# Kernel tuning notes

Measured on AMD Instinct MI355X. Metric: run time of the kernel, lower is better.

Reference implementation:

```python
import jax, jax.numpy as jnp
import numpy as np

B, D, H = 32768, 256, 8
DH = D // H
SCALE = 1.0 / float(np.sqrt(DH))
# neighbor indices: for query node i, context = the other 3 nodes (in order)
NEIGH = np.array([[1, 2, 3], [0, 2, 3], [0, 1, 3], [0, 1, 2]], dtype=np.int32)


def setup_inputs() -> dict:
    key = jax.random.key(0)
    ks = jax.random.split(key, 6)
    s = 0.02
    mk = lambda k: jax.random.normal(k, (D, D), jnp.float32) * s
    return {
        "tokens": jax.random.normal(ks[0], (B, 4, D), jnp.float32),
        "Wq": mk(ks[1]),
        "Wk": mk(ks[2]),
        "Wv": mk(ks[3]),
        "Wr": mk(ks[4]),
        "Wo": mk(ks[5]),
        "ln_g": jnp.ones((D,), jnp.float32),
        "ln_b": jnp.zeros((D,), jnp.float32),
    }


def reference(tokens, Wq, Wk, Wv, Wr, Wo, ln_g, ln_b):
    # tokens: [B,4,D]. All 4 modality queries share one GCA block (share_gca=True),
    # so we batch the 4-node complete-graph message passing into one pass.
    neigh = jnp.asarray(NEIGH)
    ctx = tokens[:, neigh]                    # [B,4,3,D]
    Q = tokens @ Wq.T                         # [B,4,D]
    K = ctx @ Wk.T                            # [B,4,3,D]
    V = ctx @ Wv.T
    R = ctx @ Wr.T
    V_eff = jax.nn.sigmoid(R) * V             # gated values
    Qh = Q.reshape(B, 4, H, DH)
    Kh = K.reshape(B, 4, 3, H, DH)
    Vh = V_eff.reshape(B, 4, 3, H, DH)
    scores = jnp.einsum('bihd,bilhd->bihl', Qh, Kh) * SCALE   # [B,4,H,3]
    attn = jax.nn.softmax(scores, axis=-1)    # dropout = identity (eval mode)
    out = jnp.einsum('bihl,bilhd->bihd', attn, Vh).reshape(B, 4, D)
    out = out @ Wo.T
    y = tokens + out                          # residual
    mu = y.mean(-1, keepdims=True)
    var = y.var(-1, keepdims=True)
    y = (y - mu) / jnp.sqrt(var + 1e-5) * ln_g + ln_b   # LayerNorm
    # attn: [B,4,H,3] -> per-query attn maps (attn[:, i] == attn for modality-i query, [B,H,1,3] squeezed)
    return y, attn
```

## Files before the change

kernel.cpp:

```cpp
#include <hip/hip_runtime.h>
#include <stdint.h>


#define D_DIM   256
#define H_NUM   8
#define DH      32
#define RT      32
#define NTHR    512
#define ROWS_TOT 131072
#define Y_SZ    33554432
#define SCALE_F 0.17677669529663687f
#define W_ELEMS 65536
#define WS_NEED (5 * W_ELEMS * 2)

#define SX_LD   264
#define SQK_LD  776
#define KOFF    256
#define VOFF    512
#define SY_LD   260

typedef __attribute__((ext_vector_type(8))) short bf16x8;
typedef __attribute__((ext_vector_type(4))) float f32x4;

__device__ __forceinline__ float b2f(uint16_t s) {
    union { uint32_t u; float f; } c; c.u = ((uint32_t)s) << 16; return c.f;
}
__device__ __forceinline__ uint16_t f2b(float f) {
    union { float f; uint32_t u; } c; c.f = f;
    return (uint16_t)((c.u + 0x7fffu + ((c.u >> 16) & 1u)) >> 16);
}
__device__ __forceinline__ bf16x8 cvt8(const float* p) {
    const float4 a = *(const float4*)p;
    const float4 b = *(const float4*)(p + 4);
    bf16x8 r;
    r[0] = (short)f2b(a.x); r[1] = (short)f2b(a.y);
    r[2] = (short)f2b(a.z); r[3] = (short)f2b(a.w);
    r[4] = (short)f2b(b.x); r[5] = (short)f2b(b.y);
    r[6] = (short)f2b(b.z); r[7] = (short)f2b(b.w);
    return r;
}

__global__ __launch_bounds__(256)
void conv_weights(const float* __restrict__ Wq, const float* __restrict__ Wk,
                  const float* __restrict__ Wv, const float* __restrict__ Wr,
                  const float* __restrict__ Wo, uint16_t* __restrict__ dst)
{
    const int m = blockIdx.x >> 6;
    const float* src = (m == 0) ? Wq : (m == 1) ? Wk : (m == 2) ? Wv
                     : (m == 3) ? Wr : Wo;
    const int base = (blockIdx.x & 63) * 1024 + threadIdx.x * 4;
    const float4 v = *(const float4*)&src[base];
    uint2 pk;
    pk.x = (uint32_t)f2b(v.x) | ((uint32_t)f2b(v.y) << 16);
    pk.y = (uint32_t)f2b(v.z) | ((uint32_t)f2b(v.w) << 16);
    *(uint2*)&dst[(size_t)m * W_ELEMS + base] = pk;
}

template<bool WBF16>
__global__ __launch_bounds__(NTHR, 4)
void cmaa_fused(const float* __restrict__ tok,
                const float* __restrict__ Wq, const float* __restrict__ Wk,
                const float* __restrict__ Wv, const float* __restrict__ Wr,
                const float* __restrict__ Wo,
                const uint16_t* __restrict__ wbf,
                const float* __restrict__ lng, const float* __restrict__ lnb,
                float* __restrict__ outp)
{
    __shared__ __align__(16) uint16_t sX [RT * SX_LD];
    __shared__ __align__(16) uint16_t sQK[RT * SQK_LD];

    const int tid  = threadIdx.x;
    const int wv   = tid >> 6;
    const int lane = tid & 63;
    const int l15  = lane & 15;
    const int quad = lane >> 4;
    const int R0   = blockIdx.x * RT;
    const int koff = blockIdx.x & 7;

    {
        const float* g = tok + (size_t)R0 * D_DIM;
        #pragma unroll
        for (int t = tid; t < RT * (D_DIM / 8); t += NTHR) {
            const int row = t >> 5, c = t & 31;
            *(bf16x8*)&sX[row * SX_LD + c * 8] = cvt8(&g[row * D_DIM + c * 8]);
        }
    }
    __syncthreads();

    {
        const int  colbase = (((wv & 3) + blockIdx.x) & 3) * 64;
        const bool qk = (wv < 4);
        const float*    WF0 = qk ? Wq : Wv;
        const float*    WF1 = qk ? Wk : Wr;
        const uint16_t* WB0 = wbf + (size_t)(qk ? 0 : 2) * W_ELEMS;
        const uint16_t* WB1 = WB0 + W_ELEMS;

        f32x4 acc[2][2][4];
        #pragma unroll
        for (int m = 0; m < 2; ++m)
            #pragma unroll
            for (int mt = 0; mt < 2; ++mt)
                #pragma unroll
                for (int nt = 0; nt < 4; ++nt)
                    acc[m][mt][nt] = (f32x4){0.f, 0.f, 0.f, 0.f};

        #pragma unroll
        for (int i = 0; i < 8; ++i) {
            const int kk = (i + koff) & 7;
            const int k0 = kk * 32;
            bf16x8 a[2];
            #pragma unroll
            for (int mt = 0; mt < 2; ++mt)
                a[mt] = *(const bf16x8*)&sX[(mt * 16 + l15) * SX_LD + k0 + quad * 8];

            bf16x8 b0[4], b1[4];
            #pragma unroll
            for (int nt = 0; nt < 4; ++nt) {
                const int wrow = colbase + nt * 16 + l15;
                if constexpr (WBF16) {
                    b0[nt] = *(const bf16x8*)&WB0[(size_t)wrow * D_DIM + k0 + quad * 8];
                    b1[nt] = *(const bf16x8*)&WB1[(size_t)wrow * D_DIM + k0 + quad * 8];
                } else {
                    b0[nt] = cvt8(&WF0[(size_t)wrow * D_DIM + k0 + quad * 8]);
                    b1[nt] = cvt8(&WF1[(size_t)wrow * D_DIM + k0 + quad * 8]);
                }
            }
            #pragma unroll
            for (int nt = 0; nt < 4; ++nt)
                #pragma unroll
                for (int mt = 0; mt < 2; ++mt)
                    acc[0][mt][nt] = __builtin_amdgcn_mfma_f32_16x16x32_bf16(a[mt], b0[nt], acc[0][mt][nt], 0, 0, 0);
            #pragma unroll
            for (int nt = 0; nt < 4; ++nt)
                #pragma unroll
                for (int mt = 0; mt < 2; ++mt)
                    acc[1][mt][nt] = __builtin_amdgcn_mfma_f32_16x16x32_bf16(a[mt], b1[nt], acc[1][mt][nt], 0, 0, 0);
        }

        if (qk) {
            #pragma unroll
            for (int mt = 0; mt < 2; ++mt)
                #pragma unroll
                for (int nt = 0; nt < 4; ++nt)
                    #pragma unroll
                    for (int r = 0; r < 4; ++r) {
                        const int row = mt * 16 + quad * 4 + r;
                        const int col = colbase + nt * 16 + l15;
                        sQK[row * SQK_LD + col]        = f2b(acc[0][mt][nt][r]);
                        sQK[row * SQK_LD + KOFF + col] = f2b(acc[1][mt][nt][r]);
                    }
        } else {
            #pragma unroll
            for (int mt = 0; mt < 2; ++mt)
                #pragma unroll
                for (int nt = 0; nt < 4; ++nt)
                    #pragma unroll
                    for (int r = 0; r < 4; ++r) {
                        const int row = mt * 16 + quad * 4 + r;
                        const int col = colbase + nt * 16 + l15;
                        const float vvv = acc[0][mt][nt][r];
                        const float rr  = acc[1][mt][nt][r];
                        const float sig = 1.f / (1.f + __expf(-rr));
                        sQK[row * SQK_LD + VOFF + col] = f2b(vvv * sig);
                    }
        }
    }
    __syncthreads();

    const int wob = ((wv + blockIdx.x) & 7) * 32;
    bf16x8 bw3[2][8];
    {
        const uint16_t* WoB = wbf + (size_t)4 * W_ELEMS;
        #pragma unroll
        for (int nt = 0; nt < 2; ++nt) {
            const int worow = wob + nt * 16 + l15;
            #pragma unroll
            for (int i = 0; i < 8; ++i) {
                const int k0 = ((i + koff) & 7) * 32;
                if constexpr (WBF16)
                    bw3[nt][i] = *(const bf16x8*)&WoB[(size_t)worow * D_DIM + k0 + quad * 8];
                else
                    bw3[nt][i] = cvt8(&Wo[(size_t)worow * D_DIM + k0 + quad * 8]);
            }
        }
    }

    {
        const int r    = tid >> 4;
        const int h    = (tid >> 1) & 7;
        const int half = tid & 1;
        const int gr = R0 + r;
        const int i  = r & 3;
        const int rb = r & ~3;
        int rn[3];
        #pragma unroll
        for (int l = 0; l < 3; ++l) { const int jj = l + (l >= i); rn[l] = rb + jj; }
        const int qoff = h * DH + half * 16;

        float q[16];
        #pragma unroll
        for (int t = 0; t < 2; ++t) {
            const bf16x8 v = *(const bf16x8*)&sQK[r * SQK_LD + qoff + t * 8];
            #pragma unroll
            for (int j = 0; j < 8; ++j) q[t * 8 + j] = b2f((uint16_t)v[j]);
        }

        float sc[3];
        #pragma unroll
        for (int l = 0; l < 3; ++l) {
            float s = 0.f;
            #pragma unroll
            for (int t = 0; t < 2; ++t) {
                const bf16x8 v = *(const bf16x8*)&sQK[rn[l] * SQK_LD + KOFF + qoff + t * 8];
                #pragma unroll
                for (int j = 0; j < 8; ++j) s += q[t * 8 + j] * b2f((uint16_t)v[j]);
            }
            s += __shfl_xor(s, 1);
            sc[l] = s * SCALE_F;
        }
        const float mx = fmaxf(sc[0], fmaxf(sc[1], sc[2]));
        const float e0 = __expf(sc[0] - mx), e1 = __expf(sc[1] - mx), e2 = __expf(sc[2] - mx);
        const float inv = 1.f / (e0 + e1 + e2);
        const float al[3] = { e0 * inv, e1 * inv, e2 * inv };

        if (half == 0) {
            float* ap = outp + Y_SZ + ((size_t)gr * H_NUM + h) * 3;
            ap[0] = al[0]; ap[1] = al[1]; ap[2] = al[2];
        }

        #pragma unroll
        for (int t = 0; t < 2; ++t) {
            float o[8] = {0.f,0.f,0.f,0.f,0.f,0.f,0.f,0.f};
            #pragma unroll
            for (int l = 0; l < 3; ++l) {
                const bf16x8 vv = *(const bf16x8*)&sQK[rn[l] * SQK_LD + VOFF + qoff + t * 8];
                #pragma unroll
                for (int j = 0; j < 8; ++j) o[j] += al[l] * b2f((uint16_t)vv[j]);
            }
            bf16x8 pk;
            #pragma unroll
            for (int j = 0; j < 8; ++j) pk[j] = (short)f2b(o[j]);
            *(bf16x8*)&sQK[r * SQK_LD + qoff + t * 8] = pk;
        }
    }
    __syncthreads();

    {
        f32x4 acc3[2][2];
        #pragma unroll
        for (int mt = 0; mt < 2; ++mt)
            #pragma unroll
            for (int nt = 0; nt < 2; ++nt)
                acc3[mt][nt] = (f32x4){0.f, 0.f, 0.f, 0.f};

        #pragma unroll
        for (int i = 0; i < 8; ++i) {
            const int k0 = ((i + koff) & 7) * 32;
            bf16x8 a[2];
            #pragma unroll
            for (int mt = 0; mt < 2; ++mt)
                a[mt] = *(const bf16x8*)&sQK[(mt * 16 + l15) * SQK_LD + k0 + quad * 8];
            #pragma unroll
            for (int nt = 0; nt < 2; ++nt)
                #pragma unroll
                for (int mt = 0; mt < 2; ++mt)
                    acc3[mt][nt] = __builtin_amdgcn_mfma_f32_16x16x32_bf16(a[mt], bw3[nt][i], acc3[mt][nt], 0, 0, 0);
        }
        __syncthreads();

        float* sY = (float*)sQK;
        #pragma unroll
        for (int mt = 0; mt < 2; ++mt)
            #pragma unroll
            for (int nt = 0; nt < 2; ++nt)
                #pragma unroll
                for (int r = 0; r < 4; ++r) {
                    const int row = mt * 16 + quad * 4 + r;
                    const int col = wob + nt * 16 + l15;
                    sY[row * SY_LD + col] = acc3[mt][nt][r] + b2f(sX[row * SX_LD + col]);
                }
    }
    __syncthreads();

    {
        const float* sY = (const float*)sQK;
        const int row = tid >> 4;
        const int sub = tid & 15;
        float vals[16];
        float s = 0.f;
        #pragma unroll
        for (int j = 0; j < 4; ++j) {
            const float4 v = *(const float4*)&sY[row * SY_LD + j * 64 + sub * 4];
            vals[j*4+0] = v.x; vals[j*4+1] = v.y; vals[j*4+2] = v.z; vals[j*4+3] = v.w;
            s += v.x + v.y + v.z + v.w;
        }
        s += __shfl_xor(s, 1); s += __shfl_xor(s, 2);
        s += __shfl_xor(s, 4); s += __shfl_xor(s, 8);
        const float mean = s * (1.f / 256.f);
        float s2 = 0.f;
        #pragma unroll
        for (int j = 0; j < 16; ++j) { const float d = vals[j] - mean; s2 += d * d; }
        s2 += __shfl_xor(s2, 1); s2 += __shfl_xor(s2, 2);
        s2 += __shfl_xor(s2, 4); s2 += __shfl_xor(s2, 8);
        const float var  = fmaxf(s2 * (1.f / 256.f), 0.f);
        const float rstd = rsqrtf(var + 1e-5f);

        float* orow = outp + (size_t)(R0 + row) * D_DIM;
        #pragma unroll
        for (int j = 0; j < 4; ++j) {
            const int col = j * 64 + sub * 4;
            const float4 g4 = *(const float4*)&lng[col];
            const float4 b4 = *(const float4*)&lnb[col];
            float4 o4;
            o4.x = (vals[j*4+0] - mean) * rstd * g4.x + b4.x;
            o4.y = (vals[j*4+1] - mean) * rstd * g4.y + b4.y;
            o4.z = (vals[j*4+2] - mean) * rstd * g4.z + b4.z;
            o4.w = (vals[j*4+3] - mean) * rstd * g4.w + b4.w;
            *(float4*)&orow[col] = o4;
        }
    }
}

extern "C" void kernel_launch(void* const* d_in, const int* in_sizes, int n_in,
                              void* d_out, int out_size, void* d_ws, size_t ws_size,
                              hipStream_t stream) {
    (void)in_sizes; (void)n_in; (void)out_size;
    const float* tok = (const float*)d_in[0];
    const float* Wq  = (const float*)d_in[1];
    const float* Wk  = (const float*)d_in[2];
    const float* Wv  = (const float*)d_in[3];
    const float* Wr  = (const float*)d_in[4];
    const float* Wo  = (const float*)d_in[5];
    const float* lng = (const float*)d_in[6];
    const float* lnb = (const float*)d_in[7];
    float* outp = (float*)d_out;
    uint16_t* wbf = (uint16_t*)d_ws;

    dim3 grid(ROWS_TOT / RT), block(NTHR);
    if (ws_size >= (size_t)WS_NEED) {
        conv_weights<<<dim3(320), dim3(256), 0, stream>>>(Wq, Wk, Wv, Wr, Wo, wbf);
        cmaa_fused<true><<<grid, block, 0, stream>>>(
            tok, Wq, Wk, Wv, Wr, Wo, wbf, lng, lnb, outp);
    } else {
        cmaa_fused<false><<<grid, block, 0, stream>>>(
            tok, Wq, Wk, Wv, Wr, Wo, wbf, lng, lnb, outp);
    }
}
```

Baseline: 511.6 us.

## Make fused kernel persistent over 64-row tiles with 1024 threads and prefetch

Switches to a persistent grid of 256 blocks of 1024 threads, each looping over 8 tiles of 64 rows. The next tile's tokens are prefetched into registers during attention and the output projection, then written to shared memory at the end of the iteration. MFMA operands are swapped so each lane holds 4 contiguous output columns, which allows packed 64-bit shared stores. This removes per-block launch and setup overhead and hides the token load latency. In exchange, 1024-thread blocks limit occupancy and register headroom, and launch_bounds(NTHR,4) now asks for 4 blocks of 1024 threads per CU.

```diff
diff --git a/kernel.cpp b/kernel.cpp
--- a/kernel.cpp
+++ b/kernel.cpp
@@ -5,8 +5,10 @@
 #define D_DIM   256
 #define H_NUM   8
 #define DH      32
-#define RT      32
-#define NTHR    512
+#define RT      64
+#define NTHR    1024
+#define NBLK    256
+#define TPB     8
 #define ROWS_TOT 131072
 #define Y_SZ    33554432
 #define SCALE_F 0.17677669529663687f
@@ -38,6 +40,12 @@
     r[4] = (short)f2b(b.x); r[5] = (short)f2b(b.y);
     r[6] = (short)f2b(b.z); r[7] = (short)f2b(b.w);
     return r;
+}
+__device__ __forceinline__ uint2 pack4(f32x4 a) {
+    uint2 p;
+    p.x = (uint32_t)f2b(a[0]) | ((uint32_t)f2b(a[1]) << 16);
+    p.y = (uint32_t)f2b(a[2]) | ((uint32_t)f2b(a[3]) << 16);
+    return p;
 }
 
 __global__ __launch_bounds__(256)
@@ -74,250 +82,265 @@
     const int lane = tid & 63;
     const int l15  = lane & 15;
     const int quad = lane >> 4;
-    const int R0   = blockIdx.x * RT;
     const int koff = blockIdx.x & 7;
 
+    const bool qk      = (wv < 8);
+    const int  colbase = (((wv & 7) + blockIdx.x) & 7) * 32;
+    const int  wob     = ((wv + blockIdx.x) & 15) * 16;
+
+    const float*    WF0 = qk ? Wq : Wv;
+    const float*    WF1 = qk ? Wk : Wr;
+    const uint16_t* WB0 = wbf + (size_t)(qk ? 0 : 2) * W_ELEMS;
+    const uint16_t* WB1 = WB0 + W_ELEMS;
+    const uint16_t* WoB = wbf + (size_t)4 * W_ELEMS;
+
+    const int sx_r0 = tid >> 5;             const int sx_c0 = tid & 31;
+    const int sx_r1 = (tid + 1024) >> 5;    const int sx_c1 = (tid + 1024) & 31;
+
+    const int tile0 = blockIdx.x * TPB;
     {
-        const float* g = tok + (size_t)R0 * D_DIM;
-        #pragma unroll
-        for (int t = tid; t < RT * (D_DIM / 8); t += NTHR) {
-            const int row = t >> 5, c = t & 31;
-            *(bf16x8*)&sX[row * SX_LD + c * 8] = cvt8(&g[row * D_DIM + c * 8]);
-        }
+        const float* g = tok + (size_t)tile0 * RT * D_DIM;
+        *(bf16x8*)&sX[sx_r0 * SX_LD + sx_c0 * 8] = cvt8(&g[sx_r0 * D_DIM + sx_c0 * 8]);
+        *(bf16x8*)&sX[sx_r1 * SX_LD + sx_c1 * 8] = cvt8(&g[sx_r1 * D_DIM + sx_c1 * 8]);
     }
     __syncthreads();
 
-    {
-        const int  colbase = (((wv & 3) + blockIdx.x) & 3) * 64;
-        const bool qk = (wv < 4);
-        const float*    WF0 = qk ? Wq : Wv;
-        const float*    WF1 = qk ? Wk : Wr;
-        const uint16_t* WB0 = wbf + (size_t)(qk ? 0 : 2) * W_ELEMS;
-        const uint16_t* WB1 = WB0 + W_ELEMS;
-
-        f32x4 acc[2][2][4];
-        #pragma unroll
-        for (int m = 0; m < 2; ++m)
-            #pragma unroll
-            for (int mt = 0; mt < 2; ++mt)
+    for (int t = 0; t < TPB; ++t) {
+        const int R0 = (tile0 + t) * RT;
+
+        {
+            f32x4 acc[2][2][4];
+            #pragma unroll
+            for (int m = 0; m < 2; ++m)
+                #pragma unroll
+                for (int ct = 0; ct < 2; ++ct)
+                    #pragma unroll
+                    for (int nt = 0; nt < 4; ++nt)
+                        acc[m][ct][nt] = (f32x4){0.f, 0.f, 0.f, 0.f};
+
+            #pragma unroll
+            for (int i = 0; i < 8; ++i) {
+                const int k0 = ((i + koff) & 7) * 32;
+                bf16x8 ax[4];
                 #pragma unroll
                 for (int nt = 0; nt < 4; ++nt)
-                    acc[m][mt][nt] = (f32x4){0.f, 0.f, 0.f, 0.f};
-
-        #pragma unroll
-        for (int i = 0; i < 8; ++i) {
-            const int kk = (i + koff) & 7;
-            const int k0 = kk * 32;
-            bf16x8 a[2];
-            #pragma unroll
-            for (int mt = 0; mt < 2; ++mt)
-                a[mt] = *(const bf16x8*)&sX[(mt * 16 + l15) * SX_LD + k0 + quad * 8];
-
-            bf16x8 b0[4], b1[4];
-            #pragma unroll
-            for (int nt = 0; nt < 4; ++nt) {
-                const int wrow = colbase + nt * 16 + l15;
-                if constexpr (WBF16) {
-                    b0[nt] = *(const bf16x8*)&WB0[(size_t)wrow * D_DIM + k0 + quad * 8];
-                    b1[nt] = *(const bf16x8*)&WB1[(size_t)wrow * D_DIM + k0 + quad * 8];
-                } else {
-                    b0[nt] = cvt8(&WF0[(size_t)wrow * D_DIM + k0 + quad * 8]);
-                    b1[nt] = cvt8(&WF1[(size_t)wrow * D_DIM + k0 + quad * 8]);
+                    ax[nt] = *(const bf16x8*)&sX[(nt * 16 + l15) * SX_LD + k0 + quad * 8];
+
+                bf16x8 b0[2], b1[2];
+                #pragma unroll
+                for (int ct = 0; ct < 2; ++ct) {
+                    const int wrow = colbase + ct * 16 + l15;
+                    if constexpr (WBF16) {
+                        b0[ct] = *(const bf16x8*)&WB0[(size_t)wrow * D_DIM + k0 + quad * 8];
+                        b1[ct] = *(const bf16x8*)&WB1[(size_t)wrow * D_DIM + k0 + quad * 8];
+                    } else {
+                        b0[ct] = cvt8(&WF0[(size_t)wrow * D_DIM + k0 + quad * 8]);
+                        b1[ct] = cvt8(&WF1[(size_t)wrow * D_DIM + k0 + quad * 8]);
+                    }
                 }
-            }
-            #pragma unroll
-            for (int nt = 0; nt < 4; ++nt)
-                #pragma unroll
-                for (int mt = 0; mt < 2; ++mt)
-                    acc[0][mt][nt] = __builtin_amdgcn_mfma_f32_16x16x32_bf16(a[mt], b0[nt], acc[0][mt][nt], 0, 0, 0);
-            #pragma unroll
-            for (int nt = 0; nt < 4; ++nt)
-                #pragma unroll
-                for (int mt = 0; mt < 2; ++mt)
-                    acc[1][mt][nt] = __builtin_amdgcn_mfma_f32_16x16x32_bf16(a[mt], b1[nt], acc[1][mt][nt], 0, 0, 0);
-        }
-
-        if (qk) {
-            #pragma unroll
-            for (int mt = 0; mt < 2; ++mt)
-                #pragma unroll
-                for (int nt = 0; nt < 4; ++nt)
-                    #pragma unroll
-                    for (int r = 0; r < 4; ++r) {
-                        const int row = mt * 16 + quad * 4 + r;
-                        const int col = colbase + nt * 16 + l15;
-                        sQK[row * SQK_LD + col]        = f2b(acc[0][mt][nt][r]);
-                        sQK[row * SQK_LD + KOFF + col] = f2b(acc[1][mt][nt][r]);
+                #pragma unroll
+                for (int ct = 0; ct < 2; ++ct)
+                    #pragma unroll
+                    for (int nt = 0; nt < 4; ++nt)
+                        acc[0][ct][nt] = __builtin_amdgcn_mfma_f32_16x16x32_bf16(b0[ct], ax[nt], acc[0][ct][nt], 0, 0, 0);
+                #pragma unroll
+                for (int ct = 0; ct < 2; ++ct)
+                    #pragma unroll
+                    for (int nt = 0; nt < 4; ++nt)
+                        acc[1][ct][nt] = __builtin_amdgcn_mfma_f32_16x16x32_bf16(b1[ct], ax[nt], acc[1][ct][nt], 0, 0, 0);
+            }
+
+            if (qk) {
+                #pragma unroll
+                for (int ct = 0; ct < 2; ++ct)
+                    #pragma unroll
+                    for (int nt = 0; nt < 4; ++nt) {
+                        const int token = nt * 16 + l15;
+                        const int cb    = colbase + ct * 16 + quad * 4;
+                        *(uint2*)&sQK[token * SQK_LD + cb]        = pack4(acc[0][ct][nt]);
+                        *(uint2*)&sQK[token * SQK_LD + KOFF + cb] = pack4(acc[1][ct][nt]);
                     }
-        } else {
-            #pragma unroll
-            for (int mt = 0; mt < 2; ++mt)
-                #pragma unroll
-                for (int nt = 0; nt < 4; ++nt)
-                    #pragma unroll
-                    for (int r = 0; r < 4; ++r) {
-                        const int row = mt * 16 + quad * 4 + r;
-                        const int col = colbase + nt * 16 + l15;
-                        const float vvv = acc[0][mt][nt][r];
-                        const float rr  = acc[1][mt][nt][r];
-                        const float sig = 1.f / (1.f + __expf(-rr));
-                        sQK[row * SQK_LD + VOFF + col] = f2b(vvv * sig);
+            } else {
+                #pragma unroll
+                for (int ct = 0; ct < 2; ++ct)
+                    #pragma unroll
+                    for (int nt = 0; nt < 4; ++nt) {
+                        const int token = nt * 16 + l15;
+                        const int cb    = colbase + ct * 16 + quad * 4;
+                        f32x4 ve;
+                        #pragma unroll
+                        for (int r = 0; r < 4; ++r) {
+                            const float sig = 1.f / (1.f + __expf(-acc[1][ct][nt][r]));
+                            ve[r] = acc[0][ct][nt][r] * sig;
+                        }
+                        *(uint2*)&sQK[token * SQK_LD + VOFF + cb] = pack4(ve);
                     }
-        }
-    }
-    __syncthreads();
-
-    const int wob = ((wv + blockIdx.x) & 7) * 32;
-    bf16x8 bw3[2][8];
-    {
-        const uint16_t* WoB = wbf + (size_t)4 * W_ELEMS;
-        #pragma unroll
-        for (int nt = 0; nt < 2; ++nt) {
-            const int worow = wob + nt * 16 + l15;
+            }
+        }
+        __syncthreads();
+
+        float4 xr0a, xr0b, xr1a, xr1b;
+        if (t + 1 < TPB) {
+            const float* gn = tok + (size_t)(R0 + RT) * D_DIM;
+            xr0a = *(const float4*)&gn[sx_r0 * D_DIM + sx_c0 * 8];
+            xr0b = *(const float4*)&gn[sx_r0 * D_DIM + sx_c0 * 8 + 4];
+            xr1a = *(const float4*)&gn[sx_r1 * D_DIM + sx_c1 * 8];
+            xr1b = *(const float4*)&gn[sx_r1 * D_DIM + sx_c1 * 8 + 4];
+        }
+        bf16x8 bw3[8];
+        {
+            const int worow = wob + l15;
             #pragma unroll
             for (int i = 0; i < 8; ++i) {
                 const int k0 = ((i + koff) & 7) * 32;
                 if constexpr (WBF16)
-                    bw3[nt][i] = *(const bf16x8*)&WoB[(size_t)worow * D_DIM + k0 + quad * 8];
+                    bw3[i] = *(const bf16x8*)&WoB[(size_t)worow * D_DIM + k0 + quad * 8];
                 else
-                    bw3[nt][i] = cvt8(&Wo[(size_t)worow * D_DIM + k0 + quad * 8]);
-            }
-        }
-    }
-
-    {
-        const int r    = tid >> 4;
-        const int h    = (tid >> 1) & 7;
-        const int half = tid & 1;
-        const int gr = R0 + r;
-        const int i  = r & 3;
-        const int rb = r & ~3;
-        int rn[3];
+                    bw3[i] = cvt8(&Wo[(size_t)worow * D_DIM + k0 + quad * 8]);
+            }
+        }
+
+        {
+            const int r    = tid >> 4;
+            const int h    = (tid >> 1) & 7;
+            const int half = tid & 1;
+            const int gr = R0 + r;
+            const int i  = r & 3;
+            const int rb = r & ~3;
+            int rn[3];
+            #pragma unroll
+            for (int l = 0; l < 3; ++l) { const int jj = l + (l >= i); rn[l] = rb + jj; }
+            const int qoff = h * DH + half * 16;
+
+            float q[16];
+            #pragma unroll
+            for (int tt = 0; tt < 2; ++tt) {
+                const bf16x8 v = *(const bf16x8*)&sQK[r * SQK_LD + qoff + tt * 8];
+                #pragma unroll
+                for (int j = 0; j < 8; ++j) q[tt * 8 + j] = b2f((uint16_t)v[j]);
+            }
+
+            float sc[3];
+            #pragma unroll
+            for (int l = 0; l < 3; ++l) {
+                float s = 0.f;
+                #pragma unroll
+                for (int tt = 0; tt < 2; ++tt) {
+                    const bf16x8 v = *(const bf16x8*)&sQK[rn[l] * SQK_LD + KOFF + qoff + tt * 8];
+                    #pragma unroll
+                    for (int j = 0; j < 8; ++j) s += q[tt * 8 + j] * b2f((uint16_t)v[j]);
+                }
+                s += __shfl_xor(s, 1);
+                sc[l] = s * SCALE_F;
+            }
+            const float mx = fmaxf(sc[0], fmaxf(sc[1], sc[2]));
+            const float e0 = __expf(sc[0] - mx), e1 = __expf(sc[1] - mx), e2 = __expf(sc[2] - mx);
+            const float inv = 1.f / (e0 + e1 + e2);
+            const float al[3] = { e0 * inv, e1 * inv, e2 * inv };
+
+            if (half == 0) {
+                float* ap = outp + Y_SZ + ((size_t)gr * H_NUM + h) * 3;
+                ap[0] = al[0]; ap[1] = al[1]; ap[2] = al[2];
+            }
+
+            #pragma unroll
+            for (int tt = 0; tt < 2; ++tt) {
+                float o[8] = {0.f,0.f,0.f,0.f,0.f,0.f,0.f,0.f};
+                #pragma unroll
+                for (int l = 0; l < 3; ++l) {
+                    const bf16x8 vv = *(const bf16x8*)&sQK[rn[l] * SQK_LD + VOFF + qoff + tt * 8];
+                    #pragma unroll
+                    for (int j = 0; j < 8; ++j) o[j] += al[l] * b2f((uint16_t)vv[j]);
+                }
+                bf16x8 pk;
+                #pragma unroll
+                for (int j = 0; j < 8; ++j) pk[j] = (short)f2b(o[j]);
+                *(bf16x8*)&sQK[r * SQK_LD + qoff + tt * 8] = pk;
+            }
+        }
+        __syncthreads();
+
+        f32x4 acc3[4];
         #pragma unroll
-        for (int l = 0; l < 3; ++l) { const int jj = l + (l >= i); rn[l] = rb + jj; }
-        const int qoff = h * DH + half * 16;
-
-        float q[16];
-        #pragma unroll
-        for (int t = 0; t < 2; ++t) {
-            const bf16x8 v = *(const bf16x8*)&sQK[r * SQK_LD + qoff + t * 8];
-            #pragma unroll
-            for (int j = 0; j < 8; ++j) q[t * 8 + j] = b2f((uint16_t)v[j]);
-        }
-
-        float sc[3];
-        #pragma unroll
-        for (int l = 0; l < 3; ++l) {
-            float s = 0.f;
-            #pragma unroll
-            for (int t = 0; t < 2; ++t) {
-                const bf16x8 v = *(const bf16x8*)&sQK[rn[l] * SQK_LD + KOFF + qoff + t * 8];
-                #pragma unroll
-                for (int j = 0; j < 8; ++j) s += q[t * 8 + j] * b2f((uint16_t)v[j]);
-            }
-            s += __shfl_xor(s, 1);
-            sc[l] = s * SCALE_F;
-        }
-        const float mx = fmaxf(sc[0], fmaxf(sc[1], sc[2]));
-        const float e0 = __expf(sc[0] - mx), e1 = __expf(sc[1] - mx), e2 = __expf(sc[2] - mx);
-        const float inv = 1.f / (e0 + e1 + e2);
-        const float al[3] = { e0 * inv, e1 * inv, e2 * inv };
-
-        if (half == 0) {
-            float* ap = outp + Y_SZ + ((size_t)gr * H_NUM + h) * 3;
-            ap[0] = al[0]; ap[1] = al[1]; ap[2] = al[2];
-        }
-
-        #pragma unroll
-        for (int t = 0; t < 2; ++t) {
-            float o[8] = {0.f,0.f,0.f,0.f,0.f,0.f,0.f,0.f};
-            #pragma unroll
-            for (int l = 0; l < 3; ++l) {
-                const bf16x8 vv = *(const bf16x8*)&sQK[rn[l] * SQK_LD + VOFF + qoff + t * 8];
-                #pragma unroll
-                for (int j = 0; j < 8; ++j) o[j] += al[l] * b2f((uint16_t)vv[j]);
-            }
-            bf16x8 pk;
-            #pragma unroll
-            for (int j = 0; j < 8; ++j) pk[j] = (short)f2b(o[j]);
-            *(bf16x8*)&sQK[r * SQK_LD + qoff + t * 8] = pk;
-        }
-    }
-    __syncthreads();
-
-    {
-        f32x4 acc3[2][2];
-        #pragma unroll
-        for (int mt = 0; mt < 2; ++mt)
-            #pragma unroll
-            for (int nt = 0; nt < 2; ++nt)
-                acc3[mt][nt] = (f32x4){0.f, 0.f, 0.f, 0.f};
+        for (int nt = 0; nt < 4; ++nt) acc3[nt] = (f32x4){0.f, 0.f, 0.f, 0.f};
 
         #pragma unroll
         for (int i = 0; i < 8; ++i) {
             const int k0 = ((i + koff) & 7) * 32;
-            bf16x8 a[2];
-            #pragma unroll
-            for (int mt = 0; mt < 2; ++mt)
-                a[mt] = *(const bf16x8*)&sQK[(mt * 16 + l15) * SQK_LD + k0 + quad * 8];
-            #pragma unroll
-            for (int nt = 0; nt < 2; ++nt)
-                #pragma unroll
-                for (int mt = 0; mt < 2; ++mt)
-                    acc3[mt][nt] = __builtin_amdgcn_mfma_f32_16x16x32_bf16(a[mt], bw3[nt][i], acc3[mt][nt], 0, 0, 0);
-        }
-        __syncthreads();
-
-        float* sY = (float*)sQK;
-        #pragma unroll
-        for (int mt = 0; mt < 2; ++mt)
-            #pragma unroll
-            for (int nt = 0; nt < 2; ++nt)
-                #pragma unroll
-                for (int r = 0; r < 4; ++r) {
-                    const int row = mt * 16 + quad * 4 + r;
-                    const int col = wob + nt * 16 + l15;
-                    sY[row * SY_LD + col] = acc3[mt][nt][r] + b2f(sX[row * SX_LD + col]);
-                }
-    }
-    __syncthreads();
-
-    {
-        const float* sY = (const float*)sQK;
-        const int row = tid >> 4;
-        const int sub = tid & 15;
-        float vals[16];
-        float s = 0.f;
-        #pragma unroll
-        for (int j = 0; j < 4; ++j) {
-            const float4 v = *(const float4*)&sY[row * SY_LD + j * 64 + sub * 4];
-            vals[j*4+0] = v.x; vals[j*4+1] = v.y; vals[j*4+2] = v.z; vals[j*4+3] = v.w;
-            s += v.x + v.y + v.z + v.w;
-        }
-        s += __shfl_xor(s, 1); s += __shfl_xor(s, 2);
-        s += __shfl_xor(s, 4); s += __shfl_xor(s, 8);
-        const float mean = s * (1.f / 256.f);
-        float s2 = 0.f;
-        #pragma unroll
-        for (int j = 0; j < 16; ++j) { const float d = vals[j] - mean; s2 += d * d; }
-        s2 += __shfl_xor(s2, 1); s2 += __shfl_xor(s2, 2);
-        s2 += __shfl_xor(s2, 4); s2 += __shfl_xor(s2, 8);
-        const float var  = fmaxf(s2 * (1.f / 256.f), 0.f);
-        const float rstd = rsqrtf(var + 1e-5f);
-
-        float* orow = outp + (size_t)(R0 + row) * D_DIM;
-        #pragma unroll
-        for (int j = 0; j < 4; ++j) {
-            const int col = j * 64 + sub * 4;
-            const float4 g4 = *(const float4*)&lng[col];
-            const float4 b4 = *(const float4*)&lnb[col];
-            float4 o4;
-            o4.x = (vals[j*4+0] - mean) * rstd * g4.x + b4.x;
-            o4.y = (vals[j*4+1] - mean) * rstd * g4.y + b4.y;
-            o4.z = (vals[j*4+2] - mean) * rstd * g4.z + b4.z;
-            o4.w = (vals[j*4+3] - mean) * rstd * g4.w + b4.w;
-            *(float4*)&orow[col] = o4;
-        }
+            bf16x8 ao[4];
+            #pragma unroll
+            for (int nt = 0; nt < 4; ++nt)
+                ao[nt] = *(const bf16x8*)&sQK[(nt * 16 + l15) * SQK_LD + k0 + quad * 8];
+            #pragma unroll
+            for (int nt = 0; nt < 4; ++nt)
+                acc3[nt] = __builtin_amdgcn_mfma_f32_16x16x32_bf16(bw3[i], ao[nt], acc3[nt], 0, 0, 0);
+        }
+        __syncthreads();
+
+        {
+            float* sY = (float*)sQK;
+            #pragma unroll
+            for (int nt = 0; nt < 4; ++nt) {
+                const int token = nt * 16 + l15;
+                const int c0    = wob + quad * 4;
+                const ushort4 xv = *(const ushort4*)&sX[token * SX_LD + c0];
+                float4 y4;
+                y4.x = acc3[nt][0] + b2f(xv.x);
+                y4.y = acc3[nt][1] + b2f(xv.y);
+                y4.z = acc3[nt][2] + b2f(xv.z);
+                y4.w = acc3[nt][3] + b2f(xv.w);
+                *(float4*)&sY[token * SY_LD + c0] = y4;
+            }
+        }
+        __syncthreads();
+
+        {
+            const float* sY = (const float*)sQK;
+            const int row = tid >> 4;
+            const int sub = tid & 15;
+            float vals[16];
+            float s = 0.f;
+            #pragma unroll
+            for (int j = 0; j < 4; ++j) {
+                const float4 v = *(const float4*)&sY[row * SY_LD + j * 64 + sub * 4];
+                vals[j*4+0] = v.x; vals[j*4+1] = v.y; vals[j*4+2] = v.z; vals[j*4+3] = v.w;
+                s += v.x + v.y + v.z + v.w;
+            }
+            s += __shfl_xor(s, 1); s += __shfl_xor(s, 2);
+            s += __shfl_xor(s, 4); s += __shfl_xor(s, 8);
+            const float mean = s * (1.f / 256.f);
+            float s2 = 0.f;
+            #pragma unroll
+            for (int j = 0; j < 16; ++j) { const float d = vals[j] - mean; s2 += d * d; }
+            s2 += __shfl_xor(s2, 1); s2 += __shfl_xor(s2, 2);
+            s2 += __shfl_xor(s2, 4); s2 += __shfl_xor(s2, 8);
+            const float var  = fmaxf(s2 * (1.f / 256.f), 0.f);
+            const float rstd = rsqrtf(var + 1e-5f);
+
+            float* orow = outp + (size_t)(R0 + row) * D_DIM;
+            #pragma unroll
+            for (int j = 0; j < 4; ++j) {
+                const int col = j * 64 + sub * 4;
+                const float4 g4 = *(const float4*)&lng[col];
+                const float4 b4 = *(const float4*)&lnb[col];
+                float4 o4;
+                o4.x = (vals[j*4+0] - mean) * rstd * g4.x + b4.x;
+                o4.y = (vals[j*4+1] - mean) * rstd * g4.y + b4.y;
+                o4.z = (vals[j*4+2] - mean) * rstd * g4.z + b4.z;
+                o4.w = (vals[j*4+3] - mean) * rstd * g4.w + b4.w;
+                *(float4*)&orow[col] = o4;
+            }
+        }
+        if (t + 1 < TPB) {
+            bf16x8 p0, p1;
+            p0[0]=(short)f2b(xr0a.x); p0[1]=(short)f2b(xr0a.y); p0[2]=(short)f2b(xr0a.z); p0[3]=(short)f2b(xr0a.w);
+            p0[4]=(short)f2b(xr0b.x); p0[5]=(short)f2b(xr0b.y); p0[6]=(short)f2b(xr0b.z); p0[7]=(short)f2b(xr0b.w);
+            p1[0]=(short)f2b(xr1a.x); p1[1]=(short)f2b(xr1a.y); p1[2]=(short)f2b(xr1a.z); p1[3]=(short)f2b(xr1a.w);
+            p1[4]=(short)f2b(xr1b.x); p1[5]=(short)f2b(xr1b.y); p1[6]=(short)f2b(xr1b.z); p1[7]=(short)f2b(xr1b.w);
+            *(bf16x8*)&sX[sx_r0 * SX_LD + sx_c0 * 8] = p0;
+            *(bf16x8*)&sX[sx_r1 * SX_LD + sx_c1 * 8] = p1;
+        }
+        __syncthreads();
     }
 }
 
@@ -336,7 +359,7 @@
     float* outp = (float*)d_out;
     uint16_t* wbf = (uint16_t*)d_ws;
 
-    dim3 grid(ROWS_TOT / RT), block(NTHR);
+    dim3 grid(NBLK), block(NTHR);
     if (ws_size >= (size_t)WS_NEED) {
         conv_weights<<<dim3(320), dim3(256), 0, stream>>>(Wq, Wk, Wv, Wr, Wo, wbf);
         cmaa_fused<true><<<grid, block, 0, stream>>>(
```

Measured after the change: 686.2 us. 1.34x slower.
